# Performance work log

Hardware: AMD Instinct MI355X
Metric: run time of the kernel (lower is better)

Reference implementation:

```python
import jax, jax.numpy as jnp
import numpy as np

EPS = 1e-8      # module eps for attention renorm
LN_EPS = 1e-5   # torch LayerNorm default


def _lin(x, w, b):
    return x @ w + b


def _ln(x, g, b):
    m = jnp.mean(x, -1, keepdims=True)
    v = jnp.var(x, -1, keepdims=True)
    return (x - m) * jax.lax.rsqrt(v + LN_EPS) * g + b


def setup_inputs() -> dict:
    key = jax.random.key(0)
    it = iter(jax.random.split(key, 48))
    B, N, IC, EC, D, S = 8, 32768, 3, 63, 128, 8
    wf = lambda i, o: jax.random.normal(next(it), (i, o), jnp.float32) / np.sqrt(i)
    bf = lambda o: jax.random.normal(next(it), (o,), jnp.float32) * 0.02
    return {
        'inputs': jax.random.normal(next(it), (B, N, IC), jnp.float32),
        'embed_pts': jax.random.normal(next(it), (B, N, EC), jnp.float32),
        'slots_mu': jax.random.normal(next(it), (1, 1, D), jnp.float32),
        'slots_sigma': jax.random.normal(next(it), (1, 1, D), jnp.float32),
        'w0': wf(IC, 64), 'b0': bf(64),
        'w1': wf(64, 32), 'b1': bf(32),
        'w2': wf(32, 32), 'b2': bf(32),
        'w3': wf(32, 32), 'b3': bf(32),
        'w4': wf(32, 32), 'b4': bf(32),
        'w5': wf(32, 32), 'b5': bf(32),
        'w7': wf(IC + EC + 32, D), 'b7': bf(D),
        'wq': wf(D, D), 'bq': bf(D),
        'wk': wf(D, D), 'bk': bf(D),
        'wv': wf(D, D), 'bv': bf(D),
        'ln_in_g': jnp.ones((D,), jnp.float32), 'ln_in_b': jnp.zeros((D,), jnp.float32),
        'ln_sl_g': jnp.ones((D,), jnp.float32), 'ln_sl_b': jnp.zeros((D,), jnp.float32),
        'ln_ff_g': jnp.ones((D,), jnp.float32), 'ln_ff_b': jnp.zeros((D,), jnp.float32),
        'gru_wih': jax.random.normal(next(it), (3 * D, D), jnp.float32) / np.sqrt(D),
        'gru_whh': jax.random.normal(next(it), (3 * D, D), jnp.float32) / np.sqrt(D),
        'gru_bih': bf(3 * D), 'gru_bhh': bf(3 * D),
        'mlp1_w': wf(D, D), 'mlp1_b': bf(D),
        'mlp2_w': wf(D, D), 'mlp2_b': bf(D),
        'num_slots': S,
    }


def reference(inputs, embed_pts, slots_mu, slots_sigma, w0, b0, w1, b1, w2, b2, w3, b3, w4, b4, w5, b5, w7, b7, wq, bq, wk, bk, wv, bv, ln_in_g, ln_in_b, ln_sl_g, ln_sl_b, ln_ff_g, ln_ff_b, gru_wih, gru_whh, gru_bih, gru_bhh, mlp1_w, mlp1_b, mlp2_w, mlp2_b, num_slots):
    # dense stack (no nonlinearities in the original)
    x = inputs
    for w, b in ((w0, b0), (w1, b1), (w2, b2), (w3, b3), (w4, b4), (w5, b5)):
        x = _lin(x, w, b)
    h = _lin(jnp.concatenate([inputs, embed_pts, x], -1), w7, b7)  # [B,N,D]
    B, N, D = h.shape
    scale = D ** -0.5

    # slot init: torch.normal(mean(mu).data, std(sigma).data) over broadcast tensors
    mu = jnp.broadcast_to(slots_mu, (B, num_slots, D))
    sg = jnp.broadcast_to(slots_sigma, (B, num_slots, D))
    mean = jax.lax.stop_gradient(jnp.mean(mu))
    std = jax.lax.stop_gradient(jnp.std(sg, ddof=1))  # torch.std is unbiased
    slots = mean + std * jax.random.normal(jax.random.key(42), (B, num_slots, D), jnp.float32)

    h = _ln(h, ln_in_g, ln_in_b)
    k = _lin(h, wk, bk)
    v = _lin(h, wv, bv)

    for _ in range(3):  # iters
        slots_prev = slots
        q = _lin(_ln(slots, ln_sl_g, ln_sl_b), wq, bq)            # [B,S,D]
        dots = jnp.einsum('bid,bjd->bij', q, k) * scale           # [B,S,N]
        attn = jax.nn.softmax(dots, axis=1) + EPS                 # softmax over slots
        attn = attn / jnp.sum(attn, -1, keepdims=True)            # renorm over inputs
        updates = jnp.einsum('bjd,bij->bid', v, attn)             # [B,S,D]
        # GRUCell (torch semantics)
        xg = updates.reshape(-1, D)
        hp = slots_prev.reshape(-1, D)
        gi = xg @ gru_wih.T + gru_bih                             # [B*S,3D]
        gh = hp @ gru_whh.T + gru_bhh
        ir, iz, inn = jnp.split(gi, 3, axis=-1)
        hr, hz, hn = jnp.split(gh, 3, axis=-1)
        r = jax.nn.sigmoid(ir + hr)
        z = jax.nn.sigmoid(iz + hz)
        n = jnp.tanh(inn + r * hn)
        slots = ((1.0 - z) * n + z * hp).reshape(B, num_slots, D)
        # residual MLP (two linears, no activation, as in source)
        m = _lin(_lin(_ln(slots, ln_ff_g, ln_ff_b), mlp1_w, mlp1_b), mlp2_w, mlp2_b)
        slots = slots + m
    return slots.reshape(B, num_slots * D)
```

## Files before the change

### kernel.cpp

```cpp
#include <hip/hip_runtime.h>


#define B_  8
#define N_  32768
#define NB_ (B_ * N_)
#define D_  128
#define S_  8

typedef unsigned int u32;
typedef unsigned short u16;
typedef __attribute__((ext_vector_type(8))) short bf16x8;
typedef __attribute__((ext_vector_type(4))) float f32x4;

__device__ inline u32 bfr1(float x) {
    u32 u = __float_as_uint(x);
    return (u + 0x7FFFu + ((u >> 16) & 1u)) >> 16;
}
__device__ inline u32 bfpack2(u32 lo, u32 hi) { return lo | (hi << 16); }

__device__ inline void threefry42(u32 c0, u32 c1, u32& o0, u32& o1) {
    const u32 k0 = 0u, k1 = 42u, k2 = 0x1BD11BDAu ^ 0u ^ 42u;
    const u32 ks[3] = {k0, k1, k2};
    u32 x0 = c0 + k0, x1 = c1 + k1;
    const int rA[4] = {13, 15, 26, 6}, rB[4] = {17, 29, 16, 24};
#pragma unroll
    for (int i = 0; i < 5; i++) {
#pragma unroll
        for (int k = 0; k < 4; k++) {
            int r = (i & 1) ? rB[k] : rA[k];
            x0 += x1;
            x1 = (x1 << r) | (x1 >> (32 - r));
            x1 ^= x0;
        }
        x0 += ks[(i + 1) % 3];
        x1 += ks[(i + 2) % 3] + (u32)(i + 1);
    }
    o0 = x0; o1 = x1;
}

__device__ inline float bits_to_normal(u32 b) {
    float f = __uint_as_float((b >> 9) | 0x3f800000u) - 1.0f;
    const float lo = -0.99999994f;
    float r = fmaxf(lo, f * 1.99999994f + lo);
    float w = -log1pf(-r * r);
    float p;
    if (w < 5.0f) {
        w -= 2.5f;
        p = 2.81022636e-08f;
        p = fmaf(p, w, 3.43273939e-07f);
        p = fmaf(p, w, -3.5233877e-06f);
        p = fmaf(p, w, -4.39150654e-06f);
        p = fmaf(p, w, 0.00021858087f);
        p = fmaf(p, w, -0.00125372503f);
        p = fmaf(p, w, -0.00417768164f);
        p = fmaf(p, w, 0.246640727f);
        p = fmaf(p, w, 1.50140941f);
    } else {
        w = sqrtf(w) - 3.0f;
        p = -0.000200214257f;
        p = fmaf(p, w, 0.000100950558f);
        p = fmaf(p, w, 0.00134934322f);
        p = fmaf(p, w, -0.00367342844f);
        p = fmaf(p, w, 0.00573950773f);
        p = fmaf(p, w, -0.0076224613f);
        p = fmaf(p, w, 0.00943887047f);
        p = fmaf(p, w, 1.00167406f);
        p = fmaf(p, w, 2.83297682f);
    }
    return 1.41421356f * (p * r);
}

__device__ inline float block128_sum(float v, float* red) {
#pragma unroll
    for (int o = 32; o; o >>= 1) v += __shfl_down(v, o);
    __syncthreads();
    if ((threadIdx.x & 63) == 0) red[threadIdx.x >> 6] = v;
    __syncthreads();
    return red[0] + red[1];
}

__device__ void emit_q(float x, int bs,
                       const float* lnsg, const float* lnsb,
                       const float* wq, const float* bq,
                       const float* wkT, const float* bk,
                       float* qt, float* qc,
                       float* shA, float* red) {
    int t = threadIdx.x;
    float m = block128_sum(x, red) * (1.0f / 128.0f);
    float e = x - m;
    float var = block128_sum(e * e, red) * (1.0f / 128.0f);
    float inv = rsqrtf(var + 1e-5f);
    __syncthreads();
    shA[t] = fmaf(e * inv, lnsg[t], lnsb[t]);
    __syncthreads();
    float q = bq[t];
#pragma unroll 4
    for (int i = 0; i < 128; i++) q = fmaf(shA[i], wq[i * 128 + t], q);
    __syncthreads();
    shA[t] = q;
    __syncthreads();
    float a2 = 0.f;
#pragma unroll 4
    for (int j = 0; j < 128; j++) a2 = fmaf(wkT[j * 128 + t], shA[j], a2);
    const float scale = 0.08838834764831845f;
    qt[bs * 128 + t] = a2 * scale;
    float pr = block128_sum(shA[t] * bk[t], red);
    if (t == 0) qc[bs] = pr * scale;
}


__global__ __launch_bounds__(256) void k0_transpose(
    const float* __restrict__ wih, const float* __restrict__ whh,
    const float* __restrict__ wk,
    float* __restrict__ wihT, float* __restrict__ whhT, float* __restrict__ wkT) {
    int idx = blockIdx.x * 256 + threadIdx.x;
    if (idx < 49152) {
        int d = idx / 384, g = idx % 384;
        wihT[idx] = wih[g * 128 + d];
    } else if (idx < 98304) {
        int o = idx - 49152;
        int d = o / 384, g = o % 384;
        whhT[o] = whh[g * 128 + d];
    } else if (idx < 114688) {
        int o = idx - 98304;
        int j = o >> 7, tcol = o & 127;
        wkT[o] = wk[tcol * 128 + j];
    }
}


__global__ __launch_bounds__(256) void k1_setup(
    const float* __restrict__ w0, const float* __restrict__ b0,
    const float* __restrict__ w1, const float* __restrict__ b1,
    const float* __restrict__ w2, const float* __restrict__ b2,
    const float* __restrict__ w3, const float* __restrict__ b3,
    const float* __restrict__ w4, const float* __restrict__ b4,
    const float* __restrict__ w5, const float* __restrict__ b5,
    const float* __restrict__ w7, const float* __restrict__ b7,
    const float* __restrict__ mu, const float* __restrict__ sg,
    float* __restrict__ Wh, float* __restrict__ bh, float* __restrict__ slots,
    u16* __restrict__ whiT) {
    __shared__ float A[192], Bt[96], bb[64], bb2[32];
    __shared__ float stats[2];
    int t = threadIdx.x;
    for (int i = t; i < 192; i += 256) A[i] = w0[i];
    for (int i = t; i < 64; i += 256) bb[i] = b0[i];
    __syncthreads();
    const float* wl[5] = {w1, w2, w3, w4, w5};
    const float* bl[5] = {b1, b2, b3, b4, b5};
    int kin = 64;
    for (int l = 0; l < 5; l++) {
        const float* w = wl[l];
        const float* bias = bl[l];
        if (t < 96) {
            int i = t / 32, j = t % 32;
            float acc = 0.f;
            for (int k = 0; k < kin; k++) acc += A[i * kin + k] * w[k * 32 + j];
            Bt[i * 32 + j] = acc;
        } else if (t < 128) {
            int j = t - 96;
            float acc = bias[j];
            for (int k = 0; k < kin; k++) acc += bb[k] * w[k * 32 + j];
            bb2[j] = acc;
        }
        __syncthreads();
        if (t < 96) A[t] = Bt[t];
        if (t < 32) bb[t] = bb2[t];
        __syncthreads();
        kin = 32;
    }
    for (int idx = t; idx < 66 * 128; idx += 256) {
        int i = idx >> 7, j = idx & 127;
        float acc = w7[idx];
        if (i < 3) {
            for (int k = 0; k < 32; k++) acc += A[i * 32 + k] * w7[(66 + k) * 128 + j];
        }
        Wh[idx] = acc;
    }
    for (int j = t; j < 128; j += 256) {
        float acc = b7[j];
        for (int k = 0; k < 32; k++) acc += bb[k] * w7[(66 + k) * 128 + j];
        bh[j] = acc;
    }
    if (t == 0) {
        float s1 = 0.f, s2 = 0.f;
        for (int d = 0; d < 128; d++) { s1 += mu[d]; s2 += sg[d]; }
        float mmu = s1 / 128.f, msg = s2 / 128.f;
        float ss = 0.f;
        for (int d = 0; d < 128; d++) { float e = sg[d] - msg; ss += e * e; }
        stats[0] = mmu;
        stats[1] = sqrtf(64.f * ss / 8191.f);
    }
    __syncthreads();
    for (int idx = t; idx < 128 * 96; idx += 256) {
        int col = idx / 96, k = idx - col * 96;
        float v = (k < 66) ? Wh[k * 128 + col] : 0.f;
        whiT[idx] = (u16)bfr1(v);
    }
    float mean = stats[0], sd = stats[1];
    for (int p = t; p < 8192; p += 256) {
        u32 o0, o1;
        threefry42(0u, (u32)p, o0, o1);
        slots[p] = fmaf(sd, bits_to_normal(o0 ^ o1), mean);
    }
}


__global__ __launch_bounds__(256) void k2_hln(
    const float* __restrict__ inputs, const float* __restrict__ embed,
    const u16* __restrict__ whiT, const float* __restrict__ bh,
    const float* __restrict__ g, const float* __restrict__ bbias,
    u16* __restrict__ hlnb) {
    __shared__ __align__(16) char smem[34816];
    __shared__ float bhl[128], gl[128], bl[128];
    int t = threadIdx.x;
    u16* ebuf = (u16*)smem;
    size_t rbase = (size_t)blockIdx.x * 128;
    for (int idx = t; idx < 384; idx += 256)
        ebuf[(idx / 3) * 104 + (idx % 3)] = (u16)bfr1(inputs[rbase * 3 + idx]);
    for (int idx = t; idx < 128 * 63; idx += 256) {
        int r = idx / 63, i = idx - r * 63;
        ebuf[r * 104 + 3 + i] = (u16)bfr1(embed[rbase * 63 + idx]);
    }
    for (int idx = t; idx < 128 * 30; idx += 256) {
        int r = idx / 30, i = idx - r * 30;
        ebuf[r * 104 + 66 + i] = 0;
    }
    if (t < 128) { bhl[t] = bh[t]; gl[t] = g[t]; bl[t] = bbias[t]; }
    __syncthreads();

    int w = t >> 6, l = t & 63;
    int c16 = l & 15, g4 = l >> 4;
    int wr0 = w * 32;
    float bhc[8], gc[8], bc[8];
#pragma unroll
    for (int nt = 0; nt < 8; nt++) {
        bhc[nt] = bhl[nt * 16 + c16];
        gc[nt] = gl[nt * 16 + c16];
        bc[nt] = bl[nt * 16 + c16];
    }
    f32x4 acc[2][8];
#pragma unroll
    for (int mi = 0; mi < 2; mi++)
#pragma unroll
        for (int nt = 0; nt < 8; nt++)
            acc[mi][nt] = (f32x4){bhc[nt], bhc[nt], bhc[nt], bhc[nt]};

#pragma unroll
    for (int kc = 0; kc < 3; kc++) {
        bf16x8 a0 = *(const bf16x8*)&ebuf[(wr0 + c16) * 104 + kc * 32 + g4 * 8];
        bf16x8 a1 = *(const bf16x8*)&ebuf[(wr0 + 16 + c16) * 104 + kc * 32 + g4 * 8];
#pragma unroll
        for (int nt = 0; nt < 8; nt++) {
            uint4 bw = *(const uint4*)(whiT + (size_t)(nt * 16 + c16) * 96 + kc * 32 + g4 * 8);
            bf16x8 bf = *(bf16x8*)&bw;
            acc[0][nt] = __builtin_amdgcn_mfma_f32_16x16x32_bf16(a0, bf, acc[0][nt], 0, 0, 0);
            acc[1][nt] = __builtin_amdgcn_mfma_f32_16x16x32_bf16(a1, bf, acc[1][nt], 0, 0, 0);
        }
    }

    __syncthreads();
    u16* T = (u16*)smem;
#pragma unroll
    for (int mi = 0; mi < 2; mi++) {
#pragma unroll
        for (int i = 0; i < 4; i++) {
            float s = 0.f;
#pragma unroll
            for (int nt = 0; nt < 8; nt++) s += acc[mi][nt][i];
            s += __shfl_xor(s, 1); s += __shfl_xor(s, 2);
            s += __shfl_xor(s, 4); s += __shfl_xor(s, 8);
            float m = s * (1.0f / 128.0f);
            float v = 0.f;
#pragma unroll
            for (int nt = 0; nt < 8; nt++) { float d = acc[mi][nt][i] - m; v = fmaf(d, d, v); }
            v += __shfl_xor(v, 1); v += __shfl_xor(v, 2);
            v += __shfl_xor(v, 4); v += __shfl_xor(v, 8);
            float inv = rsqrtf(v * (1.0f / 128.0f) + 1e-5f);
            int row = wr0 + mi * 16 + g4 * 4 + i;
#pragma unroll
            for (int nt = 0; nt < 8; nt++) {
                float val = fmaf((acc[mi][nt][i] - m) * inv, gc[nt], bc[nt]);
                T[row * 136 + nt * 16 + c16] = (u16)bfr1(val);
            }
        }
    }
    __syncthreads();
    {
        int r = t >> 1, hf = t & 1;
        const u16* Tr = T + r * 136 + hf * 64;
        u16* dst = hlnb + (rbase + r) * 128 + hf * 64;
#pragma unroll
        for (int j = 0; j < 8; j++) {
            uint4 v = *(const uint4*)(Tr + j * 8);
            *(uint4*)(dst + j * 8) = v;
        }
    }
}


__global__ __launch_bounds__(128) void k3_q(
    const float* __restrict__ slots,
    const float* __restrict__ lnsg, const float* __restrict__ lnsb,
    const float* __restrict__ wq, const float* __restrict__ bq,
    const float* __restrict__ wkT, const float* __restrict__ bk,
    float* __restrict__ qt, float* __restrict__ qc) {
    __shared__ float shA[128];
    __shared__ float red[2];
    int bs = blockIdx.x;
    float x = slots[bs * 128 + threadIdx.x];
    emit_q(x, bs, lnsg, lnsb, wq, bq, wkT, bk, qt, qc, shA, red);
}


__global__ __launch_bounds__(256) void k4_attn(
    const uint4* __restrict__ hlnb4,
    const float* __restrict__ qt, const float* __restrict__ qc,
    float* __restrict__ vecp, float* __restrict__ denp) {
    __shared__ __align__(16) u16 tiles[4][128 * 36];
    __shared__ __align__(16) u16 attnP[4][16 * 40];
    __shared__ float dlds[4][8];
    int t = threadIdx.x;
    int w = t >> 6, l = t & 63;
    int blk = blockIdx.x;
    int b = blk >> 7, slab = blk & 127;
    size_t row0 = (size_t)b * N_ + (size_t)slab * 256 + (size_t)w * 32;
    int c16 = l & 15, g = l >> 4;
    u16* tw = tiles[w];

    bf16x8 qf[4];
#pragma unroll
    for (int kc = 0; kc < 4; kc++) {
        uint4 qu = {0u, 0u, 0u, 0u};
        if (c16 < 8) {
            const float* qp = qt + b * 1024 + c16 * 128 + kc * 32 + g * 8;
            float4 qa = *(const float4*)qp;
            float4 qb = *(const float4*)(qp + 4);
            qu.x = bfpack2(bfr1(qa.x), bfr1(qa.y));
            qu.y = bfpack2(bfr1(qa.z), bfr1(qa.w));
            qu.z = bfpack2(bfr1(qb.x), bfr1(qb.y));
            qu.w = bfpack2(bfr1(qb.z), bfr1(qb.w));
        }
        qf[kc] = *(bf16x8*)&qu;
    }
    float qcv = (c16 < 8) ? qc[b * 8 + c16] : 0.f;

    f32x4 uacc[8];
#pragma unroll
    for (int nt = 0; nt < 8; nt++) uacc[nt] = (f32x4){0.f, 0.f, 0.f, 0.f};
    float denacc = 0.f;

    uint4 st[8];
#pragma unroll
    for (int mt = 0; mt < 2; mt++)
#pragma unroll
        for (int kc = 0; kc < 4; kc++)
            st[mt * 4 + kc] = hlnb4[(row0 + mt * 16 + c16) * 16 + kc * 4 + g];

    for (int tt = 0; tt < 2; tt++) {
        f32x4 dacc[2];
        dacc[0] = (f32x4){0.f, 0.f, 0.f, 0.f};
        dacc[1] = (f32x4){0.f, 0.f, 0.f, 0.f};
#pragma unroll
        for (int mt = 0; mt < 2; mt++) {
#pragma unroll
            for (int kc = 0; kc < 4; kc++) {
                uint4 au = st[mt * 4 + kc];
                dacc[mt] = __builtin_amdgcn_mfma_f32_16x16x32_bf16(*(bf16x8*)&au, qf[kc], dacc[mt], 0, 0, 0);
                int r = mt * 16 + c16;
                int d0 = kc * 32 + g * 8;
                tw[(d0 + 0) * 36 + r] = (u16)(au.x & 0xFFFF);
                tw[(d0 + 1) * 36 + r] = (u16)(au.x >> 16);
                tw[(d0 + 2) * 36 + r] = (u16)(au.y & 0xFFFF);
                tw[(d0 + 3) * 36 + r] = (u16)(au.y >> 16);
                tw[(d0 + 4) * 36 + r] = (u16)(au.z & 0xFFFF);
                tw[(d0 + 5) * 36 + r] = (u16)(au.z >> 16);
                tw[(d0 + 6) * 36 + r] = (u16)(au.w & 0xFFFF);
                tw[(d0 + 7) * 36 + r] = (u16)(au.w >> 16);
            }
        }
        if (tt == 0) {
            size_t rowB = row0 + 128;
#pragma unroll
            for (int mt = 0; mt < 2; mt++)
#pragma unroll
                for (int kc = 0; kc < 4; kc++)
                    st[mt * 4 + kc] = hlnb4[(rowB + mt * 16 + c16) * 16 + kc * 4 + g];
        }
#pragma unroll
        for (int mt = 0; mt < 2; mt++) {
            float pv[4];
#pragma unroll
            for (int r = 0; r < 4; r++) {
                float v = dacc[mt][r] + qcv;
                float mx = v;
                mx = fmaxf(mx, __shfl_xor(mx, 1));
                mx = fmaxf(mx, __shfl_xor(mx, 2));
                mx = fmaxf(mx, __shfl_xor(mx, 4));
                float e = __expf(v - mx);
                float ssum = e;
                ssum += __shfl_xor(ssum, 1);
                ssum += __shfl_xor(ssum, 2);
                ssum += __shfl_xor(ssum, 4);
                float a = (c16 < 8) ? fmaf(e, 1.0f / ssum, 1e-8f) : 0.f;
                pv[r] = a;
                denacc += a;
            }
            uint2 pw;
            pw.x = bfpack2(bfr1(pv[0]), bfr1(pv[1]));
            pw.y = bfpack2(bfr1(pv[2]), bfr1(pv[3]));
            *(uint2*)&attnP[w][c16 * 40 + mt * 16 + g * 4] = pw;
        }
        uint4 afu = *(const uint4*)&attnP[w][c16 * 40 + g * 8];
        bf16x8 af = *(bf16x8*)&afu;
#pragma unroll
        for (int nt = 0; nt < 8; nt++) {
            const u16* tp = tw + (nt * 16 + c16) * 36 + g * 8;
            uint2 blo = *(const uint2*)tp;
            uint2 bhi = *(const uint2*)(tp + 4);
            uint4 bu; bu.x = blo.x; bu.y = blo.y; bu.z = bhi.x; bu.w = bhi.y;
            uacc[nt] = __builtin_amdgcn_mfma_f32_16x16x32_bf16(af, *(bf16x8*)&bu, uacc[nt], 0, 0, 0);
        }
    }
    denacc += __shfl_xor(denacc, 16);
    denacc += __shfl_xor(denacc, 32);
    if (l < 8) dlds[w][l] = denacc;

    __syncthreads();
    float* vlds0 = (float*)&tiles[0][0];
    float* vlds1 = vlds0 + 1024;
    if (w < 2 && g < 2) {
        float* vb = (w == 0) ? vlds0 : vlds1;
#pragma unroll
        for (int nt = 0; nt < 8; nt++)
#pragma unroll
            for (int r = 0; r < 4; r++)
                vb[(g * 4 + r) * 128 + nt * 16 + c16] = uacc[nt][r];
    }
    __syncthreads();
    if (w >= 2 && g < 2) {
        float* vb = (w == 2) ? vlds0 : vlds1;
#pragma unroll
        for (int nt = 0; nt < 8; nt++)
#pragma unroll
            for (int r = 0; r < 4; r++)
                vb[(g * 4 + r) * 128 + nt * 16 + c16] += uacc[nt][r];
    }
    __syncthreads();
    float* vout = vecp + ((size_t)blk << 10);
#pragma unroll
    for (int rep = 0; rep < 4; rep++) {
        int o = rep * 256 + t;
        vout[o] = vlds0[o] + vlds1[o];
    }
    if (t < 8) denp[blk * 8 + t] = dlds[0][t] + dlds[1][t] + dlds[2][t] + dlds[3][t];
}


__device__ inline float sum512(float v, float* red8) {
#pragma unroll
    for (int o = 32; o; o >>= 1) v += __shfl_down(v, o);
    __syncthreads();
    if ((threadIdx.x & 63) == 0) red8[threadIdx.x >> 6] = v;
    __syncthreads();
    float s = 0.f;
#pragma unroll
    for (int i = 0; i < 8; i++) s += red8[i];
    return s;
}

__device__ inline float reduce4(float part, float* praw, int qq, int d) {
    __syncthreads();
    praw[qq * 128 + d] = part;
    __syncthreads();
    return praw[d] + praw[128 + d] + praw[256 + d] + praw[384 + d];
}

__global__ __launch_bounds__(512) void k5_update(
    const float* __restrict__ vecp, const float* __restrict__ denp,
    const float* __restrict__ wv, const float* __restrict__ bv,
    const float* __restrict__ wihT, const float* __restrict__ whhT,
    const float* __restrict__ bih, const float* __restrict__ bhh,
    const float* __restrict__ lnfg, const float* __restrict__ lnfb,
    const float* __restrict__ m1w, const float* __restrict__ m1b,
    const float* __restrict__ m2w, const float* __restrict__ m2b,
    float* __restrict__ slots,
    const float* __restrict__ lnsg, const float* __restrict__ lnsb,
    const float* __restrict__ wq, const float* __restrict__ bq,
    const float* __restrict__ wkT, const float* __restrict__ bk,
    float* __restrict__ qt, float* __restrict__ qc,
    float* __restrict__ out, int compute_q, int write_out) {
    __shared__ float sA[128], sB[128], sC[128], sH[128], sQ[128];
    __shared__ float praw[512];
    __shared__ float red8[8];
    __shared__ float gsc[6][512];
    int t = threadIdx.x;
    int bs = blockIdx.x;
    int b = bs >> 3, slot = bs & 7;
    int d = t & 127, qq = t >> 7;

    float dvp = (t < 128) ? denp[((size_t)(b * 128) + t) * 8 + slot] : 0.f;
    float dv = sum512(dvp, red8);

    float vs = 0.f;
    const float* vp0 = vecp + (((size_t)(b * 128 + qq * 32)) << 10) + slot * 128 + d;
#pragma unroll 8
    for (int s = 0; s < 32; s++) vs += vp0[(size_t)s << 10];
    float vtot = reduce4(vs, praw, qq, d);
    if (qq == 0) { sA[d] = vtot / dv; sC[d] = slots[bs * 128 + d]; }
    __syncthreads();

    float up = 0.f;
    {
        const float* wvp = wv + (size_t)(qq * 32) * 128 + d;
#pragma unroll 8
        for (int i = 0; i < 32; i++) up = fmaf(sA[qq * 32 + i], wvp[i * 128], up);
    }
    float updt = reduce4(up, praw, qq, d) + bv[d];
    if (qq == 0) sB[d] = updt;
    __syncthreads();

#pragma unroll 1
    for (int gx = 0; gx < 3; gx++) {
        int g = gx * 128 + d;
        float ap = 0.f, hp = 0.f;
        const float* wi = wihT + (size_t)(qq * 32) * 384 + g;
        const float* wh = whhT + (size_t)(qq * 32) * 384 + g;
#pragma unroll 8
        for (int i = 0; i < 32; i++) {
            ap = fmaf(sB[qq * 32 + i], wi[i * 384], ap);
            hp = fmaf(sC[qq * 32 + i], wh[i * 384], hp);
        }
        gsc[gx * 2][t] = ap;
        gsc[gx * 2 + 1][t] = hp;
    }
    __syncthreads();
    float gi0 = gsc[0][d] + gsc[0][128 + d] + gsc[0][256 + d] + gsc[0][384 + d] + bih[d];
    float gh0 = gsc[1][d] + gsc[1][128 + d] + gsc[1][256 + d] + gsc[1][384 + d] + bhh[d];
    float gi1 = gsc[2][d] + gsc[2][128 + d] + gsc[2][256 + d] + gsc[2][384 + d] + bih[128 + d];
    float gh1 = gsc[3][d] + gsc[3][128 + d] + gsc[3][256 + d] + gsc[3][384 + d] + bhh[128 + d];
    float gi2 = gsc[4][d] + gsc[4][128 + d] + gsc[4][256 + d] + gsc[4][384 + d] + bih[256 + d];
    float gh2 = gsc[5][d] + gsc[5][128 + d] + gsc[5][256 + d] + gsc[5][384 + d] + bhh[256 + d];
    float rg = 1.f / (1.f + expf(-(gi0 + gh0)));
    float zg = 1.f / (1.f + expf(-(gi1 + gh1)));
    float ng = tanhf(fmaf(rg, gh2, gi2));
    float hnew = (1.f - zg) * ng + zg * sC[d];
    __syncthreads();
    if (qq == 0) sH[d] = hnew;
    __syncthreads();

    float xh = (t < 128) ? sH[t] : 0.f;
    float mh = sum512(xh, red8) * (1.0f / 128.0f);
    float eh = xh - mh;
    float vh = sum512((t < 128) ? eh * eh : 0.f, red8) * (1.0f / 128.0f);
    float invh = rsqrtf(vh + 1e-5f);
    __syncthreads();
    if (t < 128) sA[t] = fmaf(eh * invh, lnfg[t], lnfb[t]);
    __syncthreads();

    float p1 = 0.f;
    {
        const float* m1p = m1w + (size_t)(qq * 32) * 128 + d;
#pragma unroll 8
        for (int i = 0; i < 32; i++) p1 = fmaf(sA[qq * 32 + i], m1p[i * 128], p1);
    }
    float m1v = reduce4(p1, praw, qq, d) + m1b[d];
    if (qq == 0) sB[d] = m1v;
    __syncthreads();

    float p2 = 0.f;
    {
        const float* m2p = m2w + (size_t)(qq * 32) * 128 + d;
#pragma unroll 8
        for (int i = 0; i < 32; i++) p2 = fmaf(sB[qq * 32 + i], m2p[i * 128], p2);
    }
    float m2v = reduce4(p2, praw, qq, d) + m2b[d];
    float snew = sH[d] + m2v;
    __syncthreads();
    if (qq == 0) {
        slots[bs * 128 + d] = snew;
        if (write_out) out[bs * 128 + d] = snew;
        sH[d] = snew;
    }
    __syncthreads();

    if (compute_q) {
        float xs = (t < 128) ? sH[t] : 0.f;
        float ms = sum512(xs, red8) * (1.0f / 128.0f);
        float es = xs - ms;
        float vs2 = sum512((t < 128) ? es * es : 0.f, red8) * (1.0f / 128.0f);
        float invs = rsqrtf(vs2 + 1e-5f);
        __syncthreads();
        if (t < 128) sA[t] = fmaf(es * invs, lnsg[t], lnsb[t]);
        __syncthreads();
        float pq = 0.f;
        {
            const float* wqp = wq + (size_t)(qq * 32) * 128 + d;
#pragma unroll 8
            for (int i = 0; i < 32; i++) pq = fmaf(sA[qq * 32 + i], wqp[i * 128], pq);
        }
        float qv = reduce4(pq, praw, qq, d) + bq[d];
        if (qq == 0) sQ[d] = qv;
        __syncthreads();
        float pa = 0.f;
        {
            const float* wkp = wkT + (size_t)(qq * 32) * 128 + d;
#pragma unroll 8
            for (int j = 0; j < 32; j++) pa = fmaf(wkp[j * 128], sQ[qq * 32 + j], pa);
        }
        const float scale = 0.08838834764831845f;
        float a2 = reduce4(pa, praw, qq, d) * scale;
        if (qq == 0) qt[bs * 128 + d] = a2;
        float xpr = (t < 128) ? sQ[t] * bk[t] : 0.f;
        float pr = sum512(xpr, red8);
        if (t == 0) qc[bs] = pr * scale;
    }
}


extern "C" void kernel_launch(void* const* d_in, const int* in_sizes, int n_in,
                              void* d_out, int out_size, void* d_ws, size_t ws_size,
                              hipStream_t stream) {
    const float* inputs = (const float*)d_in[0];
    const float* embed  = (const float*)d_in[1];
    const float* mu     = (const float*)d_in[2];
    const float* sg     = (const float*)d_in[3];
    const float* w0 = (const float*)d_in[4];  const float* b0 = (const float*)d_in[5];
    const float* w1 = (const float*)d_in[6];  const float* b1 = (const float*)d_in[7];
    const float* w2 = (const float*)d_in[8];  const float* b2 = (const float*)d_in[9];
    const float* w3 = (const float*)d_in[10]; const float* b3 = (const float*)d_in[11];
    const float* w4 = (const float*)d_in[12]; const float* b4 = (const float*)d_in[13];
    const float* w5 = (const float*)d_in[14]; const float* b5 = (const float*)d_in[15];
    const float* w7 = (const float*)d_in[16]; const float* b7 = (const float*)d_in[17];
    const float* wq = (const float*)d_in[18]; const float* bq = (const float*)d_in[19];
    const float* wk = (const float*)d_in[20]; const float* bk = (const float*)d_in[21];
    const float* wv = (const float*)d_in[22]; const float* bv = (const float*)d_in[23];
    const float* ln_in_g = (const float*)d_in[24]; const float* ln_in_b = (const float*)d_in[25];
    const float* ln_sl_g = (const float*)d_in[26]; const float* ln_sl_b = (const float*)d_in[27];
    const float* ln_ff_g = (const float*)d_in[28]; const float* ln_ff_b = (const float*)d_in[29];
    const float* gwih = (const float*)d_in[30]; const float* gwhh = (const float*)d_in[31];
    const float* gbih = (const float*)d_in[32]; const float* gbhh = (const float*)d_in[33];
    const float* m1w = (const float*)d_in[34]; const float* m1b = (const float*)d_in[35];
    const float* m2w = (const float*)d_in[36]; const float* m2b = (const float*)d_in[37];

    char* ws = (char*)d_ws;
    u16* hlnb = (u16*)ws;
    size_t off = (size_t)NB_ * 128 * 2;
    float* Wh    = (float*)(ws + off); off += 66 * 128 * 4;
    float* bh    = (float*)(ws + off); off += 128 * 4;
    float* slots = (float*)(ws + off); off += 64 * 128 * 4;
    float* qt    = (float*)(ws + off); off += 64 * 128 * 4;
    float* qc    = (float*)(ws + off); off += 64 * 4;
    float* vecp  = (float*)(ws + off); off += (size_t)1024 * 1024 * 4;
    float* denp  = (float*)(ws + off); off += 1024 * 8 * 4;
    float* wihT  = (float*)(ws + off); off += 384 * 128 * 4;
    float* whhT  = (float*)(ws + off); off += 384 * 128 * 4;
    float* wkT   = (float*)(ws + off); off += 128 * 128 * 4;
    u16* whiT    = (u16*)(ws + off); off += 128 * 96 * 2;

    k0_transpose<<<448, 256, 0, stream>>>(gwih, gwhh, wk, wihT, whhT, wkT);
    k1_setup<<<1, 256, 0, stream>>>(w0, b0, w1, b1, w2, b2, w3, b3, w4, b4, w5, b5,
                                    w7, b7, mu, sg, Wh, bh, slots, whiT);
    k2_hln<<<NB_ / 128, 256, 0, stream>>>(inputs, embed, whiT, bh,
                                          ln_in_g, ln_in_b, hlnb);
    k3_q<<<64, 128, 0, stream>>>(slots, ln_sl_g, ln_sl_b, wq, bq, wkT, bk, qt, qc);
    for (int it = 0; it < 3; it++) {
        k4_attn<<<1024, 256, 0, stream>>>((const uint4*)hlnb, qt, qc, vecp, denp);
        k5_update<<<64, 512, 0, stream>>>(vecp, denp, wv, bv, wihT, whhT, gbih, gbhh,
                                          ln_ff_g, ln_ff_b, m1w, m1b, m2w, m2b, slots,
                                          ln_sl_g, ln_sl_b, wq, bq, wkT, bk, qt, qc,
                                          (float*)d_out, (it < 2) ? 1 : 0, (it == 2) ? 1 : 0);
    }
}
```

Baseline: 261.9 us.

## Fuse first attention iteration into the hidden-LayerNorm kernel

The q projection is now computed before the input-embedding kernel, which lets k2_hln run the first iteration's slot-softmax attention and weighted-value accumulation directly on its LDS tile of normalized features. This removes one full k4_attn pass over hlnb. The cost is a longer, more register-heavy k2 kernel with extra MFMA and reduction work. There are also 2048 partial slabs of 128 rows instead of 1024, so k5 reduces twice as many partials on the first iteration, selected through a new nslab parameter.

```diff
diff --git a/kernel.cpp b/kernel.cpp
--- a/kernel.cpp
+++ b/kernel.cpp
@@ -210,12 +210,17 @@
     const float* __restrict__ inputs, const float* __restrict__ embed,
     const u16* __restrict__ whiT, const float* __restrict__ bh,
     const float* __restrict__ g, const float* __restrict__ bbias,
-    u16* __restrict__ hlnb) {
+    u16* __restrict__ hlnb,
+    const float* __restrict__ qt, const float* __restrict__ qc,
+    float* __restrict__ vecp, float* __restrict__ denp) {
     __shared__ __align__(16) char smem[34816];
+    __shared__ __align__(16) u16 attnP[4][16 * 40];
+    __shared__ float dlds[4][8];
     __shared__ float bhl[128], gl[128], bl[128];
     int t = threadIdx.x;
     u16* ebuf = (u16*)smem;
     size_t rbase = (size_t)blockIdx.x * 128;
+    int b = (int)(rbase >> 15);
     for (int idx = t; idx < 384; idx += 256)
         ebuf[(idx / 3) * 104 + (idx % 3)] = (u16)bfr1(inputs[rbase * 3 + idx]);
     for (int idx = t; idx < 128 * 63; idx += 256) {
@@ -227,11 +232,29 @@
         ebuf[r * 104 + 66 + i] = 0;
     }
     if (t < 128) { bhl[t] = bh[t]; gl[t] = g[t]; bl[t] = bbias[t]; }
-    __syncthreads();
 
     int w = t >> 6, l = t & 63;
     int c16 = l & 15, g4 = l >> 4;
     int wr0 = w * 32;
+
+    bf16x8 qf[4];
+#pragma unroll
+    for (int kc = 0; kc < 4; kc++) {
+        uint4 qu = {0u, 0u, 0u, 0u};
+        if (c16 < 8) {
+            const float* qp = qt + b * 1024 + c16 * 128 + kc * 32 + g4 * 8;
+            float4 qa = *(const float4*)qp;
+            float4 qb = *(const float4*)(qp + 4);
+            qu.x = bfpack2(bfr1(qa.x), bfr1(qa.y));
+            qu.y = bfpack2(bfr1(qa.z), bfr1(qa.w));
+            qu.z = bfpack2(bfr1(qb.x), bfr1(qb.y));
+            qu.w = bfpack2(bfr1(qb.z), bfr1(qb.w));
+        }
+        qf[kc] = *(bf16x8*)&qu;
+    }
+    float qcv = (c16 < 8) ? qc[b * 8 + c16] : 0.f;
+    __syncthreads();
+
     float bhc[8], gc[8], bc[8];
 #pragma unroll
     for (int nt = 0; nt < 8; nt++) {
@@ -296,6 +319,89 @@
             *(uint4*)(dst + j * 8) = v;
         }
     }
+    f32x4 dacc[2];
+    dacc[0] = (f32x4){0.f, 0.f, 0.f, 0.f};
+    dacc[1] = (f32x4){0.f, 0.f, 0.f, 0.f};
+#pragma unroll
+    for (int mt = 0; mt < 2; mt++) {
+#pragma unroll
+        for (int kc = 0; kc < 4; kc++) {
+            bf16x8 a = *(const bf16x8*)&T[(wr0 + mt * 16 + c16) * 136 + kc * 32 + g4 * 8];
+            dacc[mt] = __builtin_amdgcn_mfma_f32_16x16x32_bf16(a, qf[kc], dacc[mt], 0, 0, 0);
+        }
+    }
+    float denacc = 0.f;
+#pragma unroll
+    for (int mt = 0; mt < 2; mt++) {
+        float pv[4];
+#pragma unroll
+        for (int r = 0; r < 4; r++) {
+            float v = dacc[mt][r] + qcv;
+            float mx = v;
+            mx = fmaxf(mx, __shfl_xor(mx, 1));
+            mx = fmaxf(mx, __shfl_xor(mx, 2));
+            mx = fmaxf(mx, __shfl_xor(mx, 4));
+            float e = __expf(v - mx);
+            float ssum = e;
+            ssum += __shfl_xor(ssum, 1);
+            ssum += __shfl_xor(ssum, 2);
+            ssum += __shfl_xor(ssum, 4);
+            float a = (c16 < 8) ? fmaf(e, 1.0f / ssum, 1e-8f) : 0.f;
+            pv[r] = a;
+            denacc += a;
+        }
+        uint2 pw;
+        pw.x = bfpack2(bfr1(pv[0]), bfr1(pv[1]));
+        pw.y = bfpack2(bfr1(pv[2]), bfr1(pv[3]));
+        *(uint2*)&attnP[w][c16 * 40 + mt * 16 + g4 * 4] = pw;
+    }
+    denacc += __shfl_xor(denacc, 16);
+    denacc += __shfl_xor(denacc, 32);
+    if (l < 8) dlds[w][l] = denacc;
+
+    uint4 afu = *(const uint4*)&attnP[w][c16 * 40 + g4 * 8];
+    bf16x8 af = *(bf16x8*)&afu;
+    f32x4 uacc[8];
+#pragma unroll
+    for (int nt = 0; nt < 8; nt++) uacc[nt] = (f32x4){0.f, 0.f, 0.f, 0.f};
+#pragma unroll
+    for (int nt = 0; nt < 8; nt++) {
+        const u16* tp = T + (wr0 + g4 * 8) * 136 + nt * 16 + c16;
+        u32 w0 = (u32)tp[0] | ((u32)tp[136] << 16);
+        u32 w1 = (u32)tp[272] | ((u32)tp[408] << 16);
+        u32 w2 = (u32)tp[544] | ((u32)tp[680] << 16);
+        u32 w3 = (u32)tp[816] | ((u32)tp[952] << 16);
+        uint4 bu; bu.x = w0; bu.y = w1; bu.z = w2; bu.w = w3;
+        uacc[nt] = __builtin_amdgcn_mfma_f32_16x16x32_bf16(af, *(bf16x8*)&bu, uacc[nt], 0, 0, 0);
+    }
+    __syncthreads();
+    float* vlds0 = (float*)smem;
+    float* vlds1 = vlds0 + 1024;
+    if (w < 2 && g4 < 2) {
+        float* vb = (w == 0) ? vlds0 : vlds1;
+#pragma unroll
+        for (int nt = 0; nt < 8; nt++)
+#pragma unroll
+            for (int r = 0; r < 4; r++)
+                vb[(g4 * 4 + r) * 128 + nt * 16 + c16] = uacc[nt][r];
+    }
+    __syncthreads();
+    if (w >= 2 && g4 < 2) {
+        float* vb = (w == 2) ? vlds0 : vlds1;
+#pragma unroll
+        for (int nt = 0; nt < 8; nt++)
+#pragma unroll
+            for (int r = 0; r < 4; r++)
+                vb[(g4 * 4 + r) * 128 + nt * 16 + c16] += uacc[nt][r];
+    }
+    __syncthreads();
+    float* vout = vecp + ((size_t)blockIdx.x << 10);
+#pragma unroll
+    for (int rep = 0; rep < 4; rep++) {
+        int o = rep * 256 + t;
+        vout[o] = vlds0[o] + vlds1[o];
+    }
+    if (t < 8) denp[blockIdx.x * 8 + t] = dlds[0][t] + dlds[1][t] + dlds[2][t] + dlds[3][t];
 }
 
 
@@ -489,7 +595,7 @@
     const float* __restrict__ wq, const float* __restrict__ bq,
     const float* __restrict__ wkT, const float* __restrict__ bk,
     float* __restrict__ qt, float* __restrict__ qc,
-    float* __restrict__ out, int compute_q, int write_out) {
+    float* __restrict__ out, int nslab, int compute_q, int write_out) {
     __shared__ float sA[128], sB[128], sC[128], sH[128], sQ[128];
     __shared__ float praw[512];
     __shared__ float red8[8];
@@ -499,13 +605,13 @@
     int b = bs >> 3, slot = bs & 7;
     int d = t & 127, qq = t >> 7;
 
-    float dvp = (t < 128) ? denp[((size_t)(b * 128) + t) * 8 + slot] : 0.f;
+    float dvp = (t < nslab) ? denp[((size_t)(b * nslab) + t) * 8 + slot] : 0.f;
     float dv = sum512(dvp, red8);
 
+    int spq = nslab >> 2;
     float vs = 0.f;
-    const float* vp0 = vecp + (((size_t)(b * 128 + qq * 32)) << 10) + slot * 128 + d;
-#pragma unroll 8
-    for (int s = 0; s < 32; s++) vs += vp0[(size_t)s << 10];
+    const float* vp0 = vecp + (((size_t)(b * nslab + qq * spq)) << 10) + slot * 128 + d;
+    for (int s = 0; s < spq; s++) vs += vp0[(size_t)s << 10];
     float vtot = reduce4(vs, praw, qq, d);
     if (qq == 0) { sA[d] = vtot / dv; sC[d] = slots[bs * 128 + d]; }
     __syncthreads();
@@ -651,8 +757,8 @@
     float* slots = (float*)(ws + off); off += 64 * 128 * 4;
     float* qt    = (float*)(ws + off); off += 64 * 128 * 4;
     float* qc    = (float*)(ws + off); off += 64 * 4;
-    float* vecp  = (float*)(ws + off); off += (size_t)1024 * 1024 * 4;
-    float* denp  = (float*)(ws + off); off += 1024 * 8 * 4;
+    float* vecp  = (float*)(ws + off); off += (size_t)2048 * 1024 * 4;
+    float* denp  = (float*)(ws + off); off += 2048 * 8 * 4;
     float* wihT  = (float*)(ws + off); off += 384 * 128 * 4;
     float* whhT  = (float*)(ws + off); off += 384 * 128 * 4;
     float* wkT   = (float*)(ws + off); off += 128 * 128 * 4;
@@ -661,14 +767,18 @@
     k0_transpose<<<448, 256, 0, stream>>>(gwih, gwhh, wk, wihT, whhT, wkT);
     k1_setup<<<1, 256, 0, stream>>>(w0, b0, w1, b1, w2, b2, w3, b3, w4, b4, w5, b5,
                                     w7, b7, mu, sg, Wh, bh, slots, whiT);
+    k3_q<<<64, 128, 0, stream>>>(slots, ln_sl_g, ln_sl_b, wq, bq, wkT, bk, qt, qc);
     k2_hln<<<NB_ / 128, 256, 0, stream>>>(inputs, embed, whiT, bh,
-                                          ln_in_g, ln_in_b, hlnb);
-    k3_q<<<64, 128, 0, stream>>>(slots, ln_sl_g, ln_sl_b, wq, bq, wkT, bk, qt, qc);
-    for (int it = 0; it < 3; it++) {
+                                          ln_in_g, ln_in_b, hlnb, qt, qc, vecp, denp);
+    k5_update<<<64, 512, 0, stream>>>(vecp, denp, wv, bv, wihT, whhT, gbih, gbhh,
+                                      ln_ff_g, ln_ff_b, m1w, m1b, m2w, m2b, slots,
+                                      ln_sl_g, ln_sl_b, wq, bq, wkT, bk, qt, qc,
+                                      (float*)d_out, 256, 1, 0);
+    for (int it = 1; it < 3; it++) {
         k4_attn<<<1024, 256, 0, stream>>>((const uint4*)hlnb, qt, qc, vecp, denp);
         k5_update<<<64, 512, 0, stream>>>(vecp, denp, wv, bv, wihT, whhT, gbih, gbhh,
                                           ln_ff_g, ln_ff_b, m1w, m1b, m2w, m2b, slots,
                                           ln_sl_g, ln_sl_b, wq, bq, wkT, bk, qt, qc,
-                                          (float*)d_out, (it < 2) ? 1 : 0, (it == 2) ? 1 : 0);
-    }
-}
+                                          (float*)d_out, 128, (it < 2) ? 1 : 0, (it == 2) ? 1 : 0);
+    }
+}
```

Result: slower. 269.0 us (+2.7%).
